# Performance work log

Hardware: AMD Instinct MI355X
Metric: run time of the kernel (lower is better)

## Reference

```python
import jax, jax.numpy as jnp
import numpy as np

B, L, D, DFF, MODES = 16, 1536, 512, 2048, 64
KERNELS = (3, 5, 7)


def setup_inputs() -> dict:
    key = jax.random.key(0)
    ks = jax.random.split(key, 12)
    scale = 1.0 / (D * D)
    f32 = jnp.float32
    return {
        "x": jax.random.normal(ks[0], (B, L, D), f32),
        "w_real": scale * jax.random.normal(ks[1], (D, D, MODES), f32),
        "w_imag": scale * jax.random.normal(ks[2], (D, D, MODES), f32),
        "conv1_w": jax.random.normal(ks[3], (DFF, D), f32) / np.sqrt(D).astype(np.float32),
        "conv2_w": jax.random.normal(ks[4], (D, DFF), f32) / np.sqrt(DFF).astype(np.float32),
        "d1_w1": jax.random.normal(ks[5], (D // 2, D), f32) / np.sqrt(D).astype(np.float32),
        "d1_b1": jnp.zeros((D // 2,), f32),
        "d1_w2": jax.random.normal(ks[6], (len(KERNELS), D // 2), f32) / np.sqrt(D // 2).astype(np.float32),
        "d1_b2": jnp.zeros((len(KERNELS),), f32),
        "d2_w1": jax.random.normal(ks[7], (D // 2, D), f32) / np.sqrt(D).astype(np.float32),
        "d2_b1": jnp.zeros((D // 2,), f32),
        "d2_w2": jax.random.normal(ks[8], (len(KERNELS), D // 2), f32) / np.sqrt(D // 2).astype(np.float32),
        "d2_b2": jnp.zeros((len(KERNELS),), f32),
    }


def _avg_pool1d(x, k):
    # torch AvgPool1d(kernel=k, stride=1, padding=k//2), count_include_pad=True:
    # zero-pad then divide by k everywhere. x: (B, L, D) -> (B, L, D) for odd k.
    pad = k // 2
    xp = jnp.pad(x, ((0, 0), (pad, pad), (0, 0)))
    cs = jnp.pad(jnp.cumsum(xp, axis=1), ((0, 0), (1, 0), (0, 0)))
    return (cs[:, k:, :] - cs[:, :-k, :]) / k


def _moe_decomp(x, w1, b1, w2, b2):
    # trends: (B, L, D, E)
    trends = jnp.stack([_avg_pool1d(x, k) for k in KERNELS], axis=-1)
    h = jax.nn.relu(jnp.einsum("bld,hd->blh", x, w1) + b1)
    logits = jnp.einsum("blh,eh->ble", h, w2) + b2
    gates = jax.nn.softmax(logits, axis=-1)[:, :, None, :]  # (B, L, 1, E)
    x_trend = jnp.sum(trends * gates, axis=-1)
    return x - x_trend  # seasonal component


def _fourier_block(x, w_real, w_imag):
    q_ft = jnp.fft.rfft(x, axis=1)  # (B, L//2+1, D) complex
    modes = min(MODES, q_ft.shape[1])
    weights = (w_real + 1j * w_imag).astype(jnp.complex64)  # (D, D, modes)
    # batched complex matmul over the kept modes (fuses the per-mode loop)
    out_m = jnp.einsum("bmd,dem->bme", q_ft[:, :modes, :], weights[:, :, :modes])
    out_ft = jnp.zeros((x.shape[0], x.shape[1] // 2 + 1, x.shape[2]), jnp.complex64)
    out_ft = out_ft.at[:, :modes, :].set(out_m)
    return jnp.fft.irfft(out_ft, n=x.shape[1], axis=1)


def reference(x, w_real, w_imag, conv1_w, conv2_w,
              d1_w1, d1_b1, d1_w2, d1_b2,
              d2_w1, d2_b1, d2_w2, d2_b2):
    # FEB-f + residual (dropout = identity in eval)
    x = x + _fourier_block(x, w_real, w_imag)
    x = _moe_decomp(x, d1_w1, d1_b1, d1_w2, d1_b2)
    # 1x1 conv FFN == per-token linear layers
    y = jax.nn.relu(jnp.einsum("bld,fd->blf", x, conv1_w))
    y = jnp.einsum("blf,df->bld", y, conv2_w)
    res = _moe_decomp(x + y, d2_w1, d2_b1, d2_w2, d2_b2)
    return res
```

## Files before the change

kernel.cpp:

```cpp
#include <hip/hip_runtime.h>

#define B_   16
#define L_   1536
#define D_   512
#define DFF_ 2048
#define NM   64
#define HID  256

typedef short short8  __attribute__((ext_vector_type(8)));
typedef short short4v __attribute__((ext_vector_type(4)));
typedef float f32x4   __attribute__((ext_vector_type(4)));

__device__ __forceinline__ float b2f(short s) {
  unsigned int u = ((unsigned int)(unsigned short)s) << 16;
  float f; __builtin_memcpy(&f, &u, 4); return f;
}
__device__ __forceinline__ short f2b(float f) {
  unsigned int u; __builtin_memcpy(&u, &f, 4);
  u += 0x7fffu + ((u >> 16) & 1u);
  return (short)(u >> 16);
}
__device__ __forceinline__ f32x4 zero4() {
  f32x4 v; v[0]=0.f; v[1]=0.f; v[2]=0.f; v[3]=0.f; return v;
}

#define MFMA(a,b,c) __builtin_amdgcn_mfma_f32_16x16x32_bf16((a),(b),(c),0,0,0)
#define SWZ(row, grp) (((row) << 6) + ((((grp) ^ ((row) & 7))) << 3))
#define GLDS16(gp, lp) __builtin_amdgcn_global_load_lds( \
    (const __attribute__((address_space(1))) void*)(gp), \
    (__attribute__((address_space(3))) void*)(lp), 16, 0, 0)

__global__ __launch_bounds__(256) void zero_out(float* __restrict__ o, int n) {
  int i = blockIdx.x * 256 + threadIdx.x;
  if (i < n) o[i] = 0.f;
}

__global__ __launch_bounds__(256) void cvt_f32_bf16(const float* __restrict__ s,
                                                    short* __restrict__ d, int n4) {
  int i = blockIdx.x * 256 + threadIdx.x;
  if (i >= n4) return;
  f32x4 v = ((const f32x4*)s)[i];
  short4v o;
  #pragma unroll
  for (int j = 0; j < 4; ++j) o[j] = f2b(v[j]);
  ((short4v*)d)[i] = o;
}

__global__ __launch_bounds__(256) void build_tcs(short* __restrict__ tcs) {
  int i = blockIdx.x * 256 + threadIdx.x;
  if (i >= 128 * L_) return;
  int m = i / L_, l = i - m * L_;
  int mm = (m < 64) ? m : (m - 64);
  int r = (mm * l) % L_;
  float th = (float)r * (6.283185307179586f / (float)L_);
  float s, c; __sincosf(th, &s, &c);
  tcs[i] = f2b((m < 64) ? c : -s);
}
__global__ __launch_bounds__(256) void build_basis(short* __restrict__ basis) {
  int i = blockIdx.x * 256 + threadIdx.x;
  if (i >= L_ * 128) return;
  int l = i >> 7, k = i & 127;
  int m = (k < 64) ? k : (k - 64);
  int r = (m * l) % L_;
  float th = (float)r * (6.283185307179586f / (float)L_);
  float s, c; __sincosf(th, &s, &c);
  float v = (k < 64) ? ((m == 0) ? 1.f : 2.f) * (1.f / (float)L_) * c
                     : (-2.f / (float)L_) * s;
  basis[i] = f2b(v);
}

__global__ __launch_bounds__(256) void transpose_w(const float* __restrict__ w,
                                                   short* __restrict__ wt) {
  __shared__ float tile[64][17];
  int dc = blockIdx.x, e = blockIdx.y, t = threadIdx.x;
  int mBase = blockIdx.z * 16;
  {
    int dl = t >> 2, mg = t & 3;
    f32x4 v = *(const f32x4*)(w + ((long)(dc * 64 + dl) * 512 + e) * 64 + mBase + mg * 4);
    tile[dl][mg*4+0] = v[0]; tile[dl][mg*4+1] = v[1];
    tile[dl][mg*4+2] = v[2]; tile[dl][mg*4+3] = v[3];
  }
  __syncthreads();
  if (t < 128) {
    int mr = t >> 3, dg = t & 7;
    short8 o;
    #pragma unroll
    for (int j = 0; j < 8; ++j) o[j] = f2b(tile[dg * 8 + j][mr]);
    *(short8*)(wt + ((long)(mBase + mr) * 512 + e) * 512 + dc * 64 + dg * 8) = o;
  }
}

__global__ __launch_bounds__(256) void transpose_x(const float* __restrict__ x,
                                                   short* __restrict__ xt) {
  __shared__ float tile[64][65];
  int dc = blockIdx.x, lc = blockIdx.y, b = blockIdx.z, t = threadIdx.x;
  const float* xb = x + (long)b * L_ * D_;
  #pragma unroll
  for (int i = 0; i < 4; ++i) {
    int idx = i * 256 + t; int ll = idx >> 4, dg = idx & 15;
    f32x4 v = *(const f32x4*)(xb + (long)(lc * 64 + ll) * D_ + dc * 64 + dg * 4);
    tile[ll][dg*4+0] = v[0]; tile[ll][dg*4+1] = v[1];
    tile[ll][dg*4+2] = v[2]; tile[ll][dg*4+3] = v[3];
  }
  __syncthreads();
  #pragma unroll
  for (int i = 0; i < 2; ++i) {
    int idx = i * 256 + t; int dl = idx >> 3, lg = idx & 7;
    short8 o;
    #pragma unroll
    for (int j = 0; j < 8; ++j) o[j] = f2b(tile[lg * 8 + j][dl]);
    *(short8*)(xt + ((long)b * D_ + dc * 64 + dl) * L_ + lc * 64 + lg * 8) = o;
  }
}

__global__ __launch_bounds__(256) void transpose_q(const short* __restrict__ in,
                                                   short* __restrict__ out) {
  __shared__ short tile[64][72];
  int ct = blockIdx.x, rt = blockIdx.y, t = threadIdx.x;
  int r0 = rt * 64, c0 = ct * 64;
  #pragma unroll
  for (int i = 0; i < 2; ++i) {
    int idx = i * 256 + t; int r = idx >> 3, g = idx & 7;
    short8 v = *(const short8*)(in + (long)(r0 + r) * 128 + c0 + g * 8);
    #pragma unroll
    for (int j = 0; j < 8; ++j) tile[r][g * 8 + j] = v[j];
  }
  __syncthreads();
  #pragma unroll
  for (int i = 0; i < 2; ++i) {
    int idx = i * 256 + t; int c = idx >> 3, g = idx & 7;
    short8 o;
    #pragma unroll
    for (int j = 0; j < 8; ++j) o[j] = tile[g * 8 + j][c];
    *(short8*)(out + (long)(c0 + c) * 8192 + r0 + g * 8) = o;
  }
}

template<bool RELU, bool HASBIAS, bool HASRES, bool RESB>
__global__ __launch_bounds__(256) void gemm128(
    const short* __restrict__ A, long ldA, long Az,
    const short* __restrict__ W, long ldW, long Wz,
    const float* __restrict__ bias,
    const void* __restrict__ res, long ldres, long resZ,
    short* __restrict__ outB, long ldC, long Cz, int K)
{
  __shared__ short lA[128 * 64];
  __shared__ short lW[128 * 64];
  const int t = threadIdx.x, lane = t & 63, wid = t >> 6;
  const int quad = lane >> 4, l15 = lane & 15;
  const int wm = (wid & 1) * 64, wn = (wid >> 1) * 64;
  const long row0 = (long)blockIdx.x * 128, col0 = (long)blockIdx.y * 128;
  const int z = blockIdx.z;
  const short* Ab = A + (long)z * Az + row0 * ldA;
  const short* Wb = W + (long)z * Wz + col0 * ldW;

  int srcrow[4]; long srcoff[4];
  #pragma unroll
  for (int i = 0; i < 4; ++i) {
    int c = wid * 4 + i;
    int r = c * 8 + (lane >> 3);
    int g = (lane & 7) ^ (r & 7);
    srcrow[i] = r; srcoff[i] = g * 8;
  }

  f32x4 acc[4][4];
  #pragma unroll
  for (int i = 0; i < 4; ++i)
    #pragma unroll
    for (int j = 0; j < 4; ++j) acc[i][j] = zero4();

  for (int k0 = 0; k0 < K; k0 += 64) {
    __syncthreads();
    #pragma unroll
    for (int i = 0; i < 4; ++i) {
      int c = wid * 4 + i;
      GLDS16(Ab + (long)srcrow[i] * ldA + k0 + srcoff[i], lA + c * 512);
      GLDS16(Wb + (long)srcrow[i] * ldW + k0 + srcoff[i], lW + c * 512);
    }
    __syncthreads();
    #pragma unroll
    for (int ks = 0; ks < 2; ++ks) {
      int gq = ks * 4 + quad;
      short8 av[4], bv[4];
      #pragma unroll
      for (int mi = 0; mi < 4; ++mi) av[mi] = *(const short8*)&lA[SWZ(wm + mi * 16 + l15, gq)];
      #pragma unroll
      for (int ni = 0; ni < 4; ++ni) bv[ni] = *(const short8*)&lW[SWZ(wn + ni * 16 + l15, gq)];
      #pragma unroll
      for (int mi = 0; mi < 4; ++mi)
        #pragma unroll
        for (int ni = 0; ni < 4; ++ni)
          acc[mi][ni] = MFMA(av[mi], bv[ni], acc[mi][ni]);
    }
  }
  #pragma unroll
  for (int ni = 0; ni < 4; ++ni) {
    long col = col0 + wn + ni * 16 + l15;
    float bvv = HASBIAS ? bias[col] : 0.f;
    #pragma unroll
    for (int mi = 0; mi < 4; ++mi) {
      #pragma unroll
      for (int r = 0; r < 4; ++r) {
        long row = row0 + wm + mi * 16 + quad * 4 + r;
        float v = acc[mi][ni][r];
        if (HASBIAS) v += bvv;
        if (RELU)    v = fmaxf(v, 0.f);
        if (HASRES) {
          long ro = (long)z * resZ + row * ldres + col;
          v += RESB ? b2f(((const short*)res)[ro]) : ((const float*)res)[ro];
        }
        outB[(long)z * Cz + row * ldC + col] = f2b(v);
      }
    }
  }
}

__global__ __launch_bounds__(256) void mode_gemm(
    const short* __restrict__ qr, const short* __restrict__ qi,
    const short* __restrict__ wr, const short* __restrict__ wi,
    short* __restrict__ outm)
{
  __shared__ short lqr[16 * 64], lqi[16 * 64], lwr[64 * 64], lwi[64 * 64];
  const int m = blockIdx.x, en = blockIdx.y;
  const int t = threadIdx.x, lane = t & 63, wid = t >> 6;
  const int quad = lane >> 4, l15 = lane & 15;
  const short* qrb = qr + (long)m * (B_ * D_);
  const short* qib = qi + (long)m * (B_ * D_);
  const short* wrb = wr + (long)m * (D_ * D_) + (long)en * 64 * D_;
  const short* wib = wi + (long)m * (D_ * D_) + (long)en * 64 * D_;
  f32x4 accr = zero4(), acci = zero4();
  for (int k0 = 0; k0 < D_; k0 += 64) {
    __syncthreads();
    {
      int idx = t & 127; int r = idx >> 3, cg = idx & 7;
      const short* src = (t < 128 ? qrb : qib) + r * D_ + k0 + cg * 8;
      short* dst = (t < 128) ? lqr : lqi;
      *(short8*)&dst[SWZ(r, cg)] = *(const short8*)src;
    }
    #pragma unroll
    for (int i = 0; i < 4; ++i) {
      int idx = i * 256 + t;
      int which = idx >> 9, idx2 = idx & 511;
      int r = idx2 >> 3, cg = idx2 & 7;
      const short* src = (which ? wib : wrb) + r * D_ + k0 + cg * 8;
      short* dst = which ? lwi : lwr;
      *(short8*)&dst[SWZ(r, cg)] = *(const short8*)src;
    }
    __syncthreads();
    #pragma unroll
    for (int ks = 0; ks < 2; ++ks) {
      int gq = ks * 4 + quad;
      short8 ar = *(const short8*)&lqr[SWZ(l15, gq)];
      short8 ai = *(const short8*)&lqi[SWZ(l15, gq)];
      short8 br = *(const short8*)&lwr[SWZ(wid * 16 + l15, gq)];
      short8 bi = *(const short8*)&lwi[SWZ(wid * 16 + l15, gq)];
      short8 nai;
      #pragma unroll
      for (int j = 0; j < 8; ++j) nai[j] = (short)(ai[j] ^ (short)0x8000);
      accr = MFMA(ar, br, accr);
      accr = MFMA(nai, bi, accr);
      acci = MFMA(ar, bi, acci);
      acci = MFMA(ai, br, acci);
    }
  }
  #pragma unroll
  for (int r = 0; r < 4; ++r) {
    int bb = quad * 4 + r;
    long e = (long)en * 64 + wid * 16 + l15;
    long base = ((long)bb * D_ + e) * 128 + m;
    outm[base]      = f2b(accr[r]);
    outm[base + 64] = f2b(acci[r]);
  }
}

__global__ __launch_bounds__(256) void gates_kernel(
    const short* __restrict__ h, const float* __restrict__ w2,
    const float* __restrict__ b2, float* __restrict__ g, int rows)
{
  int wid = threadIdx.x >> 6, lane = threadIdx.x & 63;
  int row = blockIdx.x * 4 + wid;
  if (row >= rows) return;
  const short* hr = h + (long)row * HID;
  short4v hh = *(const short4v*)(hr + lane * 4);
  float hv[4];
  #pragma unroll
  for (int j = 0; j < 4; ++j) hv[j] = b2f(hh[j]);
  float lg[3];
  #pragma unroll
  for (int e = 0; e < 3; ++e) {
    const float* wrow = w2 + e * HID + lane * 4;
    float p = hv[0] * wrow[0] + hv[1] * wrow[1] + hv[2] * wrow[2] + hv[3] * wrow[3];
    #pragma unroll
    for (int off = 32; off >= 1; off >>= 1) p += __shfl_xor(p, off);
    lg[e] = p + b2[e];
  }
  float mx = fmaxf(lg[0], fmaxf(lg[1], lg[2]));
  float e0 = __expf(lg[0] - mx), e1 = __expf(lg[1] - mx), e2 = __expf(lg[2] - mx);
  float inv = 1.f / (e0 + e1 + e2);
  float gv = (lane == 0) ? e0 * inv : (lane == 1) ? e1 * inv : e2 * inv;
  if (lane < 3) g[(long)row * 3 + lane] = gv;
}

template<bool OUTF, bool WRITEB>
__global__ __launch_bounds__(512) void combine_kernel(
    const short* __restrict__ xin, const float* __restrict__ g,
    float* __restrict__ outf, short* __restrict__ outb)
{
  int lc = blockIdx.x, b = blockIdx.y, d = threadIdx.x;
  int l0 = lc * 64;
  const short* xb = xin + (long)b * L_ * D_ + d;
  const float* gb = g + (long)b * L_ * 3;
  float win[7];
  #pragma unroll
  for (int j = 0; j < 6; ++j) {
    int l = l0 - 3 + j;
    win[j] = (l >= 0 && l < L_) ? b2f(xb[(long)l * D_]) : 0.f;
  }
  for (int i = 0; i < 64; ++i) {
    int lcn = l0 + i;
    int lr = lcn + 3;
    win[6] = (lr < L_) ? b2f(xb[(long)lr * D_]) : 0.f;
    float s3 = win[2] + win[3] + win[4];
    float s5 = s3 + win[1] + win[5];
    float s7 = s5 + win[0] + win[6];
    float g0 = gb[lcn * 3 + 0], g1 = gb[lcn * 3 + 1], g2 = gb[lcn * 3 + 2];
    float trend = g0 * s3 * (1.f / 3.f) + g1 * s5 * (1.f / 5.f) + g2 * s7 * (1.f / 7.f);
    float v = win[3] - trend;
    long o = ((long)b * L_ + lcn) * D_ + d;
    if (OUTF)   outf[o] = v;
    if (WRITEB) outb[o] = f2b(v);
    #pragma unroll
    for (int j = 0; j < 6; ++j) win[j] = win[j + 1];
  }
}

extern "C" void kernel_launch(void* const* d_in, const int* in_sizes, int n_in,
                              void* d_out, int out_size, void* d_ws, size_t ws_size,
                              hipStream_t stream) {
  const float* x       = (const float*)d_in[0];
  const float* w_real  = (const float*)d_in[1];
  const float* w_imag  = (const float*)d_in[2];
  const float* conv1_w = (const float*)d_in[3];
  const float* conv2_w = (const float*)d_in[4];
  const float* d1_w1   = (const float*)d_in[5];
  const float* d1_b1   = (const float*)d_in[6];
  const float* d1_w2   = (const float*)d_in[7];
  const float* d1_b2   = (const float*)d_in[8];
  const float* d2_w1   = (const float*)d_in[9];
  const float* d2_b1   = (const float*)d_in[10];
  const float* d2_w2   = (const float*)d_in[11];
  const float* d2_b2   = (const float*)d_in[12];
  float* OUT = (float*)d_out;

  const size_t REQUIRED = 106954752;
  if (ws_size < REQUIRED) {
    zero_out<<<(out_size + 255) / 256, 256, 0, stream>>>(OUT, out_size);
    return;
  }

  char* ws = (char*)d_ws;
  short* C1WB  = (short*)(ws + 0);
  short* C2WB  = (short*)(ws + 2097152);
  short* D1W1B = (short*)(ws + 4194304);
  short* D2W1B = (short*)(ws + 4456448);
  short* TCS   = (short*)(ws + 4718592);
  short* BASIS = (short*)(ws + 5111808);
  float* G     = (float*)(ws + 5505024);
  short* XT    = (short*)(ws + 6291456);
  short* QRI   = XT;
  short* Y1C   = XT;
  short* QT    = (short*)(ws + 31457280);
  short* ZB    = QT;
  short* OUTM  = (short*)(ws + 33554432);
  short* WTR   = (short*)(ws + 35651584);
  short* X1B   = WTR;
  short* WTI   = (short*)(ws + 69206016);
  short* X2B   = WTI;
  short* H     = (short*)(ws + 94371840);

  cvt_f32_bf16<<<(262144 + 255) / 256, 256, 0, stream>>>(conv1_w, C1WB, 262144);
  cvt_f32_bf16<<<(262144 + 255) / 256, 256, 0, stream>>>(conv2_w, C2WB, 262144);
  cvt_f32_bf16<<<(32768 + 255) / 256, 256, 0, stream>>>(d1_w1, D1W1B, 32768);
  cvt_f32_bf16<<<(32768 + 255) / 256, 256, 0, stream>>>(d2_w1, D2W1B, 32768);
  build_tcs<<<(128 * L_ + 255) / 256, 256, 0, stream>>>(TCS);
  build_basis<<<(L_ * 128 + 255) / 256, 256, 0, stream>>>(BASIS);
  transpose_w<<<dim3(8, 512, 4), 256, 0, stream>>>(w_real, WTR);
  transpose_w<<<dim3(8, 512, 4), 256, 0, stream>>>(w_imag, WTI);
  transpose_x<<<dim3(8, 24, 16), 256, 0, stream>>>(x, XT);

  gemm128<false, false, false, false><<<dim3(64, 1, 1), 256, 0, stream>>>(
      XT, L_, 0, TCS, L_, 0, nullptr, nullptr, 0, 0, QT, 128, 0, L_);
  transpose_q<<<dim3(2, 128), 256, 0, stream>>>(QT, QRI);

  mode_gemm<<<dim3(64, 8), 256, 0, stream>>>(QRI, QRI + 64 * B_ * D_, WTR, WTI, OUTM);

  gemm128<false, false, true, false><<<dim3(12, 4, 16), 256, 0, stream>>>(
      BASIS, 128, 0, OUTM, 128, (long)D_ * 128, nullptr,
      x, D_, (long)L_ * D_, X1B, D_, (long)L_ * D_, 128);

  gemm128<true, true, false, false><<<dim3(192, 2, 1), 256, 0, stream>>>(
      X1B, D_, 0, D1W1B, D_, 0, d1_b1, nullptr, 0, 0, H, HID, 0, D_);
  gates_kernel<<<6144, 256, 0, stream>>>(H, d1_w2, d1_b2, G, B_ * L_);
  combine_kernel<false, true><<<dim3(24, 16), 512, 0, stream>>>(X1B, G, nullptr, X2B);

  for (int rc = 0; rc < 4; ++rc) {
    const short* Ain = X2B + (long)rc * 6144 * D_;
    gemm128<true, false, false, false><<<dim3(48, 16, 1), 256, 0, stream>>>(
        Ain, D_, 0, C1WB, D_, 0, nullptr, nullptr, 0, 0, Y1C, DFF_, 0, D_);
    gemm128<false, false, true, true><<<dim3(48, 4, 1), 256, 0, stream>>>(
        Y1C, DFF_, 0, C2WB, DFF_, 0, nullptr, Ain, D_, 0,
        ZB + (long)rc * 6144 * D_, D_, 0, DFF_);
  }

  gemm128<true, true, false, false><<<dim3(192, 2, 1), 256, 0, stream>>>(
      ZB, D_, 0, D2W1B, D_, 0, d2_b1, nullptr, 0, 0, H, HID, 0, D_);
  gates_kernel<<<6144, 256, 0, stream>>>(H, d2_w2, d2_b2, G, B_ * L_);
  combine_kernel<true, false><<<dim3(24, 16), 512, 0, stream>>>(ZB, G, OUT, nullptr);
}
```

Before: 699.6 us.

## Add 64x64 GEMM for small GEMMs and enlarge FFN chunks with in-place residual output

Adds a gemm64 kernel with 64x64 tiles and uses it for the Fourier projection GEMM and both gate-hidden GEMMs, which raises block count so more CUs are occupied on these small-N problems. The FFN loop now runs in 1 or 2 large chunks instead of 4, sized by available workspace, and writes the second GEMM's output in place over its input, removing the separate ZB buffer. The in-place write relies on each output tile reading only its own residual element, and the larger chunks need more workspace.

```diff
diff --git a/kernel.cpp b/kernel.cpp
--- a/kernel.cpp
+++ b/kernel.cpp
@@ -133,6 +133,77 @@
     #pragma unroll
     for (int j = 0; j < 8; ++j) o[j] = tile[g * 8 + j][c];
     *(short8*)(out + (long)(c0 + c) * 8192 + r0 + g * 8) = o;
+  }
+}
+
+template<bool RELU, bool HASBIAS>
+__global__ __launch_bounds__(256) void gemm64(
+    const short* __restrict__ A, long ldA,
+    const short* __restrict__ W, long ldW,
+    const float* __restrict__ bias,
+    short* __restrict__ outB, long ldC, int K)
+{
+  __shared__ short lA[64 * 64];
+  __shared__ short lW[64 * 64];
+  const int t = threadIdx.x, lane = t & 63, wid = t >> 6;
+  const int quad = lane >> 4, l15 = lane & 15;
+  const int wm = (wid & 1) * 32, wn = (wid >> 1) * 32;
+  const long row0 = (long)blockIdx.x * 64, col0 = (long)blockIdx.y * 64;
+  const short* Ab = A + row0 * ldA;
+  const short* Wb = W + col0 * ldW;
+
+  int srcrow[2]; long srcoff[2];
+  #pragma unroll
+  for (int i = 0; i < 2; ++i) {
+    int c = wid * 2 + i;
+    int r = c * 8 + (lane >> 3);
+    int g = (lane & 7) ^ (r & 7);
+    srcrow[i] = r; srcoff[i] = g * 8;
+  }
+
+  f32x4 acc[2][2];
+  #pragma unroll
+  for (int i = 0; i < 2; ++i)
+    #pragma unroll
+    for (int j = 0; j < 2; ++j) acc[i][j] = zero4();
+
+  for (int k0 = 0; k0 < K; k0 += 64) {
+    __syncthreads();
+    #pragma unroll
+    for (int i = 0; i < 2; ++i) {
+      int c = wid * 2 + i;
+      GLDS16(Ab + (long)srcrow[i] * ldA + k0 + srcoff[i], lA + c * 512);
+      GLDS16(Wb + (long)srcrow[i] * ldW + k0 + srcoff[i], lW + c * 512);
+    }
+    __syncthreads();
+    #pragma unroll
+    for (int ks = 0; ks < 2; ++ks) {
+      int gq = ks * 4 + quad;
+      short8 a0 = *(const short8*)&lA[SWZ(wm + l15, gq)];
+      short8 a1 = *(const short8*)&lA[SWZ(wm + 16 + l15, gq)];
+      short8 b0 = *(const short8*)&lW[SWZ(wn + l15, gq)];
+      short8 b1 = *(const short8*)&lW[SWZ(wn + 16 + l15, gq)];
+      acc[0][0] = MFMA(a0, b0, acc[0][0]);
+      acc[0][1] = MFMA(a0, b1, acc[0][1]);
+      acc[1][0] = MFMA(a1, b0, acc[1][0]);
+      acc[1][1] = MFMA(a1, b1, acc[1][1]);
+    }
+  }
+  #pragma unroll
+  for (int ni = 0; ni < 2; ++ni) {
+    long col = col0 + wn + ni * 16 + l15;
+    float bvv = HASBIAS ? bias[col] : 0.f;
+    #pragma unroll
+    for (int mi = 0; mi < 2; ++mi) {
+      #pragma unroll
+      for (int r = 0; r < 4; ++r) {
+        long row = row0 + wm + mi * 16 + quad * 4 + r;
+        float v = acc[mi][ni][r];
+        if (HASBIAS) v += bvv;
+        if (RELU)    v = fmaxf(v, 0.f);
+        outB[row * ldC + col] = f2b(v);
+      }
+    }
   }
 }
 
@@ -352,11 +423,12 @@
   const float* d2_b2   = (const float*)d_in[12];
   float* OUT = (float*)d_out;
 
-  const size_t REQUIRED = 106954752;
-  if (ws_size < REQUIRED) {
+  const size_t REQ_BIG = 144703488, REQ_SMALL = 98566144;
+  if (ws_size < REQ_SMALL) {
     zero_out<<<(out_size + 255) / 256, 256, 0, stream>>>(OUT, out_size);
     return;
   }
+  const bool big = (ws_size >= REQ_BIG);
 
   char* ws = (char*)d_ws;
   short* C1WB  = (short*)(ws + 0);
@@ -368,15 +440,14 @@
   float* G     = (float*)(ws + 5505024);
   short* XT    = (short*)(ws + 6291456);
   short* QRI   = XT;
-  short* Y1C   = XT;
+  short* Y1    = XT;
   short* QT    = (short*)(ws + 31457280);
-  short* ZB    = QT;
   short* OUTM  = (short*)(ws + 33554432);
   short* WTR   = (short*)(ws + 35651584);
   short* X1B   = WTR;
   short* WTI   = (short*)(ws + 69206016);
-  short* X2B   = WTI;
-  short* H     = (short*)(ws + 94371840);
+  short* X2B   = (short*)(ws + (big ? 106954752 : 60817408));
+  short* H     = (short*)(ws + (big ? 132120576 : 85983232));
 
   cvt_f32_bf16<<<(262144 + 255) / 256, 256, 0, stream>>>(conv1_w, C1WB, 262144);
   cvt_f32_bf16<<<(262144 + 255) / 256, 256, 0, stream>>>(conv2_w, C2WB, 262144);
@@ -388,8 +459,8 @@
   transpose_w<<<dim3(8, 512, 4), 256, 0, stream>>>(w_imag, WTI);
   transpose_x<<<dim3(8, 24, 16), 256, 0, stream>>>(x, XT);
 
-  gemm128<false, false, false, false><<<dim3(64, 1, 1), 256, 0, stream>>>(
-      XT, L_, 0, TCS, L_, 0, nullptr, nullptr, 0, 0, QT, 128, 0, L_);
+  gemm64<false, false><<<dim3(128, 2), 256, 0, stream>>>(
+      XT, L_, TCS, L_, nullptr, QT, 128, L_);
   transpose_q<<<dim3(2, 128), 256, 0, stream>>>(QT, QRI);
 
   mode_gemm<<<dim3(64, 8), 256, 0, stream>>>(QRI, QRI + 64 * B_ * D_, WTR, WTI, OUTM);
@@ -398,22 +469,25 @@
       BASIS, 128, 0, OUTM, 128, (long)D_ * 128, nullptr,
       x, D_, (long)L_ * D_, X1B, D_, (long)L_ * D_, 128);
 
-  gemm128<true, true, false, false><<<dim3(192, 2, 1), 256, 0, stream>>>(
-      X1B, D_, 0, D1W1B, D_, 0, d1_b1, nullptr, 0, 0, H, HID, 0, D_);
+  gemm64<true, true><<<dim3(384, 4), 256, 0, stream>>>(
+      X1B, D_, D1W1B, D_, d1_b1, H, HID, D_);
   gates_kernel<<<6144, 256, 0, stream>>>(H, d1_w2, d1_b2, G, B_ * L_);
   combine_kernel<false, true><<<dim3(24, 16), 512, 0, stream>>>(X1B, G, nullptr, X2B);
 
-  for (int rc = 0; rc < 4; ++rc) {
-    const short* Ain = X2B + (long)rc * 6144 * D_;
-    gemm128<true, false, false, false><<<dim3(48, 16, 1), 256, 0, stream>>>(
-        Ain, D_, 0, C1WB, D_, 0, nullptr, nullptr, 0, 0, Y1C, DFF_, 0, D_);
-    gemm128<false, false, true, true><<<dim3(48, 4, 1), 256, 0, stream>>>(
-        Y1C, DFF_, 0, C2WB, DFF_, 0, nullptr, Ain, D_, 0,
-        ZB + (long)rc * 6144 * D_, D_, 0, DFF_);
-  }
-
-  gemm128<true, true, false, false><<<dim3(192, 2, 1), 256, 0, stream>>>(
-      ZB, D_, 0, D2W1B, D_, 0, d2_b1, nullptr, 0, 0, H, HID, 0, D_);
+  {
+    const int nchunk = big ? 1 : 2;
+    const long rows = big ? 24576 : 12288;
+    for (int rc = 0; rc < nchunk; ++rc) {
+      short* Ain = X2B + (long)rc * rows * D_;
+      gemm128<true, false, false, false><<<dim3(rows / 128, 16, 1), 256, 0, stream>>>(
+          Ain, D_, 0, C1WB, D_, 0, nullptr, nullptr, 0, 0, Y1, DFF_, 0, D_);
+      gemm128<false, false, true, true><<<dim3(rows / 128, 4, 1), 256, 0, stream>>>(
+          Y1, DFF_, 0, C2WB, DFF_, 0, nullptr, Ain, D_, 0, Ain, D_, 0, DFF_);
+    }
+  }
+
+  gemm64<true, true><<<dim3(384, 4), 256, 0, stream>>>(
+      X2B, D_, D2W1B, D_, d2_b1, H, HID, D_);
   gates_kernel<<<6144, 256, 0, stream>>>(H, d2_w2, d2_b2, G, B_ * L_);
-  combine_kernel<true, false><<<dim3(24, 16), 512, 0, stream>>>(ZB, G, OUT, nullptr);
-}
+  combine_kernel<true, false><<<dim3(24, 16), 512, 0, stream>>>(X2B, G, OUT, nullptr);
+}
```

Result: faster. 634.0 us (-9.4%).
